# Performance work log

Hardware: AMD Instinct MI355X
Metric: run time of the kernel (lower is better)

Reference implementation:

```python
import jax, jax.numpy as jnp
import numpy as np

N = 100000
E = 1600000
D_IN = 128
HID = 128
OUT = 64


def _sage_conv(x, edge_index, W_l, W_r, b, num_nodes):
    # PyG SAGEConv (aggr='mean'): out = lin_l(mean_{j in N(i)} x_j) + lin_r(x_i)
    src, dst = edge_index[0], edge_index[1]
    msgs = x[src]  # [E, d] gather from source nodes
    summed = jax.ops.segment_sum(msgs, dst, num_segments=num_nodes)  # [N, d]
    cnt = jax.ops.segment_sum(jnp.ones((msgs.shape[0],), x.dtype), dst, num_segments=num_nodes)
    agg = summed / jnp.maximum(cnt, 1.0)[:, None]  # mean; isolated nodes -> 0
    return agg @ W_l + b + x @ W_r


def setup_inputs() -> dict:
    key = jax.random.key(0)
    ks = jax.random.split(key, 8)
    x = jax.random.normal(ks[0], (N, D_IN), dtype=jnp.float32)
    edge_index = jax.random.randint(ks[1], (2, E), 0, N, dtype=jnp.int64)
    s1 = 1.0 / np.sqrt(D_IN)
    s2 = 1.0 / np.sqrt(HID)
    W_l1 = jax.random.uniform(ks[2], (D_IN, HID), jnp.float32, -s1, s1)
    W_r1 = jax.random.uniform(ks[3], (D_IN, HID), jnp.float32, -s1, s1)
    b1 = jnp.zeros((HID,), jnp.float32)
    W_l2 = jax.random.uniform(ks[4], (HID, OUT), jnp.float32, -s2, s2)
    W_r2 = jax.random.uniform(ks[5], (HID, OUT), jnp.float32, -s2, s2)
    b2 = jnp.zeros((OUT,), jnp.float32)
    return {"x": x, "edge_index": edge_index, "W_l1": W_l1, "W_r1": W_r1,
            "b1": b1, "W_l2": W_l2, "W_r2": W_r2, "b2": b2}


def reference(x, edge_index, W_l1, W_r1, b1, W_l2, W_r2, b2):
    h = _sage_conv(x, edge_index, W_l1, W_r1, b1, N)
    h = jax.nn.relu(h)
    out = _sage_conv(h, edge_index, W_l2, W_r2, b2, N)
    return out
```

## Files before the change

kernel.cpp:

```cpp
#include <hip/hip_runtime.h>
#include <hip/hip_fp16.h>

typedef __attribute__((ext_vector_type(8))) short bf16x8;
typedef __attribute__((ext_vector_type(4))) float f32x4;

__device__ __forceinline__ f32x4 mfma16(bf16x8 a, bf16x8 b, f32x4 c) {
    return __builtin_amdgcn_mfma_f32_16x16x32_bf16(a, b, c, 0, 0, 0);
}

__device__ __forceinline__ unsigned short bf16_rte(float f) {
    unsigned int u = __float_as_uint(f);
    unsigned int r = (u + 0x7FFFu + ((u >> 16) & 1u)) >> 16;
    return (unsigned short)r;
}
__device__ __forceinline__ float bf16_f(unsigned short h) {
    return __uint_as_float(((unsigned int)h) << 16);
}

__device__ __forceinline__ void split8h(bf16x8 raw, bf16x8& hi, bf16x8& lo) {
#pragma unroll
    for (int j = 0; j < 8; ++j) {
        float f = __half2float(__ushort_as_half((unsigned short)raw[j]));
        unsigned short h = bf16_rte(f);
        hi[j] = (short)h;
        lo[j] = (short)bf16_rte(f - bf16_f(h));
    }
}

__global__ __launch_bounds__(256) void k_prep(
    const float* __restrict__ Wl1, const float* __restrict__ Wr1,
    const float* __restrict__ Wl2, const float* __restrict__ Wr2,
    unsigned short* __restrict__ w1ah, unsigned short* __restrict__ w1al,
    unsigned short* __restrict__ w1bh, unsigned short* __restrict__ w1bl,
    unsigned short* __restrict__ w2ah, unsigned short* __restrict__ w2al,
    unsigned short* __restrict__ w2bh, unsigned short* __restrict__ w2bl,
    const float* __restrict__ x, unsigned short* __restrict__ x16,
    int* __restrict__ bcnt, int nb, int total8) {
    int b = blockIdx.x;
    int t = threadIdx.x;
    if (b < 192) {
        const float* W;
        unsigned short *hi, *lo;
        int F, e;
        if (b < 64)       { W = Wl1; hi = w1ah; lo = w1al; F = 128; e = b * 256 + t; }
        else if (b < 128) { W = Wr1; hi = w1bh; lo = w1bl; F = 128; e = (b - 64) * 256 + t; }
        else if (b < 160) { W = Wl2; hi = w2ah; lo = w2al; F = 64;  e = (b - 128) * 256 + t; }
        else              { W = Wr2; hi = w2bh; lo = w2bl; F = 64;  e = (b - 160) * 256 + t; }
        if (e >= 128 * F) return;
        int col = e >> 7, k = e & 127;
        float v = W[(size_t)k * F + col];
        unsigned short h = bf16_rte(v);
        hi[e] = h;
        lo[e] = bf16_rte(v - bf16_f(h));
    } else if (b == 192) {
        for (int i = t; i < nb; i += 256) bcnt[i] = 0;
    } else {
        int i = (b - 193) * 256 + t;
        if (i >= total8) return;
        const float4* xp = (const float4*)x + (size_t)i * 2;
        float4 a = xp[0], bb = xp[1];
        bf16x8 o;
        o[0] = (short)__half_as_ushort(__float2half_rn(a.x));
        o[1] = (short)__half_as_ushort(__float2half_rn(a.y));
        o[2] = (short)__half_as_ushort(__float2half_rn(a.z));
        o[3] = (short)__half_as_ushort(__float2half_rn(a.w));
        o[4] = (short)__half_as_ushort(__float2half_rn(bb.x));
        o[5] = (short)__half_as_ushort(__float2half_rn(bb.y));
        o[6] = (short)__half_as_ushort(__float2half_rn(bb.z));
        o[7] = (short)__half_as_ushort(__float2half_rn(bb.w));
        *(bf16x8*)&x16[(size_t)i * 8] = o;
    }
}


#define MAXNB 1024

__global__ __launch_bounds__(256) void k_bcount(
    const int* __restrict__ dst, int* __restrict__ bcnt, int E, int chunk, int nb) {
    __shared__ int h[MAXNB];
    int t = threadIdx.x;
    for (int i = t; i < nb; i += 256) h[i] = 0;
    __syncthreads();
    int base = blockIdx.x * chunk;
    int end = min(base + chunk, E);
    for (int i = base + t; i < end; i += 256) atomicAdd(&h[dst[i] >> 7], 1);
    __syncthreads();
    for (int i = t; i < nb; i += 256)
        if (h[i]) atomicAdd(&bcnt[i], h[i]);
}

__global__ void k_bscan(const int* __restrict__ bcnt, int* __restrict__ boff,
                        int* __restrict__ bcur, int nb) {
    __shared__ int sh[1024];
    int t = threadIdx.x;
    int v = (t < nb) ? bcnt[t] : 0;
    sh[t] = v;
    __syncthreads();
    for (int off = 1; off < 1024; off <<= 1) {
        int u = (t >= off) ? sh[t - off] : 0;
        __syncthreads();
        sh[t] += u;
        __syncthreads();
    }
    if (t < nb) {
        int ex = sh[t] - v;
        boff[t] = ex;
        bcur[t] = ex;
    }
}

__global__ __launch_bounds__(256) void k_bscatter(
    const int* __restrict__ src, const int* __restrict__ dst,
    int* __restrict__ bcur, int2* __restrict__ pairs, int E, int chunk, int nb) {
    __shared__ int h[MAXNB];
    __shared__ int curs[MAXNB];
    int t = threadIdx.x;
    for (int i = t; i < nb; i += 256) h[i] = 0;
    __syncthreads();
    int base = blockIdx.x * chunk;
    int end = min(base + chunk, E);
    for (int i = base + t; i < end; i += 256) atomicAdd(&h[dst[i] >> 7], 1);
    __syncthreads();
    for (int i = t; i < nb; i += 256)
        curs[i] = h[i] ? atomicAdd(&bcur[i], h[i]) : 0;
    __syncthreads();
    for (int i = base + t; i < end; i += 256) {
        int d = dst[i];
        int p = atomicAdd(&curs[d >> 7], 1);
        pairs[p] = make_int2(d, src[i]);
    }
}

__global__ __launch_bounds__(256) void k_build(
    const int2* __restrict__ pairs, const int* __restrict__ boff,
    int* __restrict__ csr, int* __restrict__ start, int* __restrict__ deg,
    int n, int nb, int E) {
    __shared__ int scnt[128];
    __shared__ int soff[128];
    __shared__ int cur[128];
    int b = blockIdx.x;
    int t = threadIdx.x;
    int base = boff[b];
    int end = (b + 1 < nb) ? boff[b + 1] : E;
    if (t < 128) scnt[t] = 0;
    __syncthreads();
    for (int i = base + t; i < end; i += 256) {
        int2 e = pairs[i];
        atomicAdd(&scnt[e.x & 127], 1);
    }
    __syncthreads();
    if (t < 128) soff[t] = scnt[t];
    __syncthreads();
    for (int off = 1; off < 128; off <<= 1) {
        int val = 0;
        if (t < 128 && t >= off) val = soff[t - off];
        __syncthreads();
        if (t < 128) soff[t] += val;
        __syncthreads();
    }
    if (t < 128) {
        int c = scnt[t];
        int ex = soff[t] - c;
        int node = b * 128 + t;
        if (node < n) {
            start[node] = base + ex;
            deg[node] = c;
        }
        cur[t] = base + ex;
    }
    __syncthreads();
    for (int i = base + t; i < end; i += 256) {
        int2 e = pairs[i];
        int p = atomicAdd(&cur[e.x & 127], 1);
        csr[p] = e.y;
    }
}


#define SR 40

__global__ __launch_bounds__(256, 2) void gemm1f(
    const unsigned short* __restrict__ X0h, const unsigned short* __restrict__ X1h,
    const unsigned short* __restrict__ W0H, const unsigned short* __restrict__ W0L,
    const unsigned short* __restrict__ W1H, const unsigned short* __restrict__ W1L,
    const float* __restrict__ bias, unsigned short* __restrict__ dstH, int n) {
    constexpr int FOUT = 128;
    constexpr int CT = 2;
    __shared__ unsigned short aHi[4][64 * SR], aLo[4][64 * SR];

    int t = threadIdx.x;
    int wv = t >> 6, l = t & 63, q = l >> 4, nl = l & 15;
    int wc = wv * (FOUT / 4);
    int node0 = blockIdx.x * 64;
    int sn = t >> 2, q4 = t & 3;
    int gn = min(node0 + sn, n - 1);

    bf16x8 s1r[4];
    {
        const unsigned short* p = X1h + (size_t)gn * 128 + q4 * 8;
#pragma unroll
        for (int c = 0; c < 4; ++c) s1r[c] = *(const bf16x8*)(p + c * 32);
    }
    bf16x8 w1h0[CT], w1l0[CT];
#pragma unroll
    for (int uu = 0; uu < CT; ++uu) {
        int base = (wc + uu * 16 + nl) * 128 + q * 8;
        w1h0[uu] = *(const bf16x8*)&W1H[base];
        w1l0[uu] = *(const bf16x8*)&W1L[base];
    }

    {
        const unsigned short* p = X0h + (size_t)gn * 128 + q4 * 8;
        bf16x8 r[4];
#pragma unroll
        for (int c = 0; c < 4; ++c) r[c] = *(const bf16x8*)(p + c * 32);
        int base = sn * SR + q4 * 8;
#pragma unroll
        for (int c = 0; c < 4; ++c) {
            bf16x8 hi, lo;
            split8h(r[c], hi, lo);
            *(bf16x8*)&aHi[c][base] = hi;
            *(bf16x8*)&aLo[c][base] = lo;
        }
    }

    f32x4 acc[4][CT];
#pragma unroll
    for (int a = 0; a < 4; ++a)
#pragma unroll
        for (int b = 0; b < CT; ++b) acc[a][b] = (f32x4){0.f, 0.f, 0.f, 0.f};

    bf16x8 wh[2][CT], wl[2][CT];
#pragma unroll
    for (int uu = 0; uu < CT; ++uu) {
        int base = (wc + uu * 16 + nl) * 128 + q * 8;
        wh[0][uu] = *(const bf16x8*)&W0H[base];
        wl[0][uu] = *(const bf16x8*)&W0L[base];
    }
    __syncthreads();

#pragma unroll
    for (int c = 0; c < 4; ++c) {
        if (c < 3) {
#pragma unroll
            for (int uu = 0; uu < CT; ++uu) {
                int base = (wc + uu * 16 + nl) * 128 + (c + 1) * 32 + q * 8;
                wh[(c + 1) & 1][uu] = *(const bf16x8*)&W0H[base];
                wl[(c + 1) & 1][uu] = *(const bf16x8*)&W0L[base];
            }
        }
        bf16x8 ah[4], al[4];
#pragma unroll
        for (int tt = 0; tt < 4; ++tt) {
            int off = (tt * 16 + nl) * SR + q * 8;
            ah[tt] = *(const bf16x8*)&aHi[c][off];
            al[tt] = *(const bf16x8*)&aLo[c][off];
        }
        int cb = c & 1;
#pragma unroll
        for (int tt = 0; tt < 4; ++tt)
#pragma unroll
            for (int uu = 0; uu < CT; ++uu) {
                f32x4 a = acc[tt][uu];
                a = mfma16(al[tt], wh[cb][uu], a);
                a = mfma16(ah[tt], wl[cb][uu], a);
                a = mfma16(ah[tt], wh[cb][uu], a);
                acc[tt][uu] = a;
            }
    }
    __syncthreads();

    {
        int base = sn * SR + q4 * 8;
#pragma unroll
        for (int c = 0; c < 4; ++c) {
            bf16x8 hi, lo;
            split8h(s1r[c], hi, lo);
            *(bf16x8*)&aHi[c][base] = hi;
            *(bf16x8*)&aLo[c][base] = lo;
        }
    }
#pragma unroll
    for (int uu = 0; uu < CT; ++uu) { wh[0][uu] = w1h0[uu]; wl[0][uu] = w1l0[uu]; }
    __syncthreads();

#pragma unroll
    for (int c = 0; c < 4; ++c) {
        if (c < 3) {
#pragma unroll
            for (int uu = 0; uu < CT; ++uu) {
                int base = (wc + uu * 16 + nl) * 128 + (c + 1) * 32 + q * 8;
                wh[(c + 1) & 1][uu] = *(const bf16x8*)&W1H[base];
                wl[(c + 1) & 1][uu] = *(const bf16x8*)&W1L[base];
            }
        }
        bf16x8 ah[4], al[4];
#pragma unroll
        for (int tt = 0; tt < 4; ++tt) {
            int off = (tt * 16 + nl) * SR + q * 8;
            ah[tt] = *(const bf16x8*)&aHi[c][off];
            al[tt] = *(const bf16x8*)&aLo[c][off];
        }
        int cb = c & 1;
#pragma unroll
        for (int tt = 0; tt < 4; ++tt)
#pragma unroll
            for (int uu = 0; uu < CT; ++uu) {
                f32x4 a = acc[tt][uu];
                a = mfma16(al[tt], wh[cb][uu], a);
                a = mfma16(ah[tt], wl[cb][uu], a);
                a = mfma16(ah[tt], wh[cb][uu], a);
                acc[tt][uu] = a;
            }
    }
    __syncthreads();

    unsigned short* tb = &aHi[0][0];
#pragma unroll
    for (int uu = 0; uu < CT; ++uu) {
        int col = wc + uu * 16 + nl;
        float bv = bias[col];
#pragma unroll
        for (int tt = 0; tt < 4; ++tt)
#pragma unroll
            for (int r = 0; r < 4; ++r) {
                float vv = fmaxf(acc[tt][uu][r] + bv, 0.f);
                tb[(tt * 16 + q * 4 + r) * 136 + col] =
                    __half_as_ushort(__float2half_rn(vv));
            }
    }
    __syncthreads();
    int node = node0 + sn;
    if (node < n) {
        const unsigned short* sp = tb + sn * 136 + q4 * 32;
        unsigned short* dp = dstH + (size_t)node * 128 + q4 * 32;
#pragma unroll
        for (int i = 0; i < 4; ++i) *(bf16x8*)(dp + i * 8) = *(const bf16x8*)(sp + i * 8);
    }
}

__global__ __launch_bounds__(256, 2) void gemm2d(
    const unsigned short* __restrict__ H,
    const unsigned short* __restrict__ WaH, const unsigned short* __restrict__ WaL,
    const unsigned short* __restrict__ WbH, const unsigned short* __restrict__ WbL,
    const float* __restrict__ bias, unsigned short* __restrict__ p16,
    float* __restrict__ outF, int n) {
    constexpr int CT = 2;
    __shared__ unsigned short aHi[4][64 * SR], aLo[4][64 * SR];

    int t = threadIdx.x;
    int wv = t >> 6, l = t & 63, q = l >> 4, nl = l & 15;
    int ysel = wv >> 1;
    int wc = (wv & 1) * 32;
    int node0 = blockIdx.x * 64;
    int sn = t >> 2, q4 = t & 3;
    int gn = min(node0 + sn, n - 1);
    const unsigned short* WH = ysel ? WbH : WaH;
    const unsigned short* WL = ysel ? WbL : WaL;

    {
        const unsigned short* p = H + (size_t)gn * 128 + q4 * 8;
        bf16x8 r[4];
#pragma unroll
        for (int c = 0; c < 4; ++c) r[c] = *(const bf16x8*)(p + c * 32);
        int base = sn * SR + q4 * 8;
#pragma unroll
        for (int c = 0; c < 4; ++c) {
            bf16x8 hi, lo;
            split8h(r[c], hi, lo);
            *(bf16x8*)&aHi[c][base] = hi;
            *(bf16x8*)&aLo[c][base] = lo;
        }
    }

    f32x4 acc[4][CT];
#pragma unroll
    for (int a = 0; a < 4; ++a)
#pragma unroll
        for (int b = 0; b < CT; ++b) acc[a][b] = (f32x4){0.f, 0.f, 0.f, 0.f};

    bf16x8 wh[2][CT], wl[2][CT];
#pragma unroll
    for (int uu = 0; uu < CT; ++uu) {
        int base = (wc + uu * 16 + nl) * 128 + q * 8;
        wh[0][uu] = *(const bf16x8*)&WH[base];
        wl[0][uu] = *(const bf16x8*)&WL[base];
    }
    __syncthreads();

#pragma unroll
    for (int c = 0; c < 4; ++c) {
        if (c < 3) {
#pragma unroll
            for (int uu = 0; uu < CT; ++uu) {
                int base = (wc + uu * 16 + nl) * 128 + (c + 1) * 32 + q * 8;
                wh[(c + 1) & 1][uu] = *(const bf16x8*)&WH[base];
                wl[(c + 1) & 1][uu] = *(const bf16x8*)&WL[base];
            }
        }
        bf16x8 ah[4], al[4];
#pragma unroll
        for (int tt = 0; tt < 4; ++tt) {
            int off = (tt * 16 + nl) * SR + q * 8;
            ah[tt] = *(const bf16x8*)&aHi[c][off];
            al[tt] = *(const bf16x8*)&aLo[c][off];
        }
        int cb = c & 1;
#pragma unroll
        for (int tt = 0; tt < 4; ++tt)
#pragma unroll
            for (int uu = 0; uu < CT; ++uu) {
                f32x4 a = acc[tt][uu];
                a = mfma16(al[tt], wh[cb][uu], a);
                a = mfma16(ah[tt], wl[cb][uu], a);
                a = mfma16(ah[tt], wh[cb][uu], a);
                acc[tt][uu] = a;
            }
    }
    __syncthreads();

    unsigned short* tbu = &aHi[0][0];
    float* tbf = (float*)&aLo[0][0];
#pragma unroll
    for (int uu = 0; uu < CT; ++uu) {
        int col = wc + uu * 16 + nl;
        if (ysel) {
            float bv = bias[col];
#pragma unroll
            for (int tt = 0; tt < 4; ++tt)
#pragma unroll
                for (int r = 0; r < 4; ++r)
                    tbf[(tt * 16 + q * 4 + r) * 68 + col] = acc[tt][uu][r] + bv;
        } else {
#pragma unroll
            for (int tt = 0; tt < 4; ++tt)
#pragma unroll
                for (int r = 0; r < 4; ++r)
                    tbu[(tt * 16 + q * 4 + r) * 72 + col] =
                        __half_as_ushort(__float2half_rn(acc[tt][uu][r]));
        }
    }
    __syncthreads();
    int node = node0 + sn;
    if (node < n) {
        const unsigned short* spu = tbu + sn * 72 + q4 * 16;
        unsigned short* dpu = p16 + (size_t)node * 64 + q4 * 16;
        *(bf16x8*)dpu = *(const bf16x8*)spu;
        *(bf16x8*)(dpu + 8) = *(const bf16x8*)(spu + 8);
        const float* spf = tbf + sn * 68 + q4 * 16;
        float* dpf = outF + (size_t)node * 64 + q4 * 16;
#pragma unroll
        for (int i = 0; i < 4; ++i) *(float4*)(dpf + i * 4) = *(const float4*)(spf + i * 4);
    }
}

__global__ __launch_bounds__(256) void aggF(
    const unsigned short* __restrict__ tab, const int* __restrict__ csr,
    const int* __restrict__ start, const int* __restrict__ deg,
    unsigned short* __restrict__ outm, int n) {
    int gid = blockIdx.x * blockDim.x + threadIdx.x;
    int wave = gid >> 6, lane = gid & 63;
    int sub = lane >> 4, fl = lane & 15;
    int node = wave * 4 + sub;
    if (node >= n) return;
    int s = start[node], d = deg[node];
    float4 A0 = {0.f, 0.f, 0.f, 0.f}, A1 = {0.f, 0.f, 0.f, 0.f};
    int j = 0;
    if (d >= 4) {
        int i0 = csr[s], i1 = csr[s + 1], i2 = csr[s + 2], i3 = csr[s + 3];
        for (; j + 8 <= d; j += 4) {
            int n0 = csr[s + j + 4], n1 = csr[s + j + 5];
            int n2 = csr[s + j + 6], n3 = csr[s + j + 7];
            uint4 r0 = ((const uint4*)(tab + (size_t)i0 * 128))[fl];
            uint4 r1 = ((const uint4*)(tab + (size_t)i1 * 128))[fl];
            uint4 r2 = ((const uint4*)(tab + (size_t)i2 * 128))[fl];
            uint4 r3 = ((const uint4*)(tab + (size_t)i3 * 128))[fl];
#pragma unroll
            for (int e = 0; e < 4; ++e) {
                uint4 r = e == 0 ? r0 : (e == 1 ? r1 : (e == 2 ? r2 : r3));
                float2 v0 = __half22float2(*(const __half2*)&r.x);
                float2 v1 = __half22float2(*(const __half2*)&r.y);
                float2 v2 = __half22float2(*(const __half2*)&r.z);
                float2 v3 = __half22float2(*(const __half2*)&r.w);
                A0.x += v0.x; A0.y += v0.y; A0.z += v1.x; A0.w += v1.y;
                A1.x += v2.x; A1.y += v2.y; A1.z += v3.x; A1.w += v3.y;
            }
            i0 = n0; i1 = n1; i2 = n2; i3 = n3;
        }
        {
            uint4 r0 = ((const uint4*)(tab + (size_t)i0 * 128))[fl];
            uint4 r1 = ((const uint4*)(tab + (size_t)i1 * 128))[fl];
            uint4 r2 = ((const uint4*)(tab + (size_t)i2 * 128))[fl];
            uint4 r3 = ((const uint4*)(tab + (size_t)i3 * 128))[fl];
#pragma unroll
            for (int e = 0; e < 4; ++e) {
                uint4 r = e == 0 ? r0 : (e == 1 ? r1 : (e == 2 ? r2 : r3));
                float2 v0 = __half22float2(*(const __half2*)&r.x);
                float2 v1 = __half22float2(*(const __half2*)&r.y);
                float2 v2 = __half22float2(*(const __half2*)&r.z);
                float2 v3 = __half22float2(*(const __half2*)&r.w);
                A0.x += v0.x; A0.y += v0.y; A0.z += v1.x; A0.w += v1.y;
                A1.x += v2.x; A1.y += v2.y; A1.z += v3.x; A1.w += v3.y;
            }
            j += 4;
        }
    }
    for (; j < d; ++j) {
        uint4 r = ((const uint4*)(tab + (size_t)csr[s + j] * 128))[fl];
        float2 v0 = __half22float2(*(const __half2*)&r.x);
        float2 v1 = __half22float2(*(const __half2*)&r.y);
        float2 v2 = __half22float2(*(const __half2*)&r.z);
        float2 v3 = __half22float2(*(const __half2*)&r.w);
        A0.x += v0.x; A0.y += v0.y; A0.z += v1.x; A0.w += v1.y;
        A1.x += v2.x; A1.y += v2.y; A1.z += v3.x; A1.w += v3.y;
    }
    float inv = 1.0f / (float)max(d, 1);
    __half2 h0 = __floats2half2_rn(A0.x * inv, A0.y * inv);
    __half2 h1 = __floats2half2_rn(A0.z * inv, A0.w * inv);
    __half2 h2 = __floats2half2_rn(A1.x * inv, A1.y * inv);
    __half2 h3 = __floats2half2_rn(A1.z * inv, A1.w * inv);
    uint4 w;
    w.x = *(unsigned int*)&h0;
    w.y = *(unsigned int*)&h1;
    w.z = *(unsigned int*)&h2;
    w.w = *(unsigned int*)&h3;
    *(uint4*)&outm[(size_t)node * 128 + fl * 8] = w;
}

__global__ __launch_bounds__(256) void aggP(
    const unsigned short* __restrict__ tab, const int* __restrict__ csr,
    const int* __restrict__ start, const int* __restrict__ deg,
    float* __restrict__ outF, int n) {
    int gid = blockIdx.x * blockDim.x + threadIdx.x;
    int wave = gid >> 6, lane = gid & 63;
    int sub = lane >> 4, fl = lane & 15;
    int node = wave * 4 + sub;
    if (node >= n) return;
    int s = start[node], d = deg[node];
    float4 A = {0.f, 0.f, 0.f, 0.f};
    int j = 0;
    if (d >= 4) {
        int i0 = csr[s], i1 = csr[s + 1], i2 = csr[s + 2], i3 = csr[s + 3];
        for (; j + 8 <= d; j += 4) {
            int n0 = csr[s + j + 4], n1 = csr[s + j + 5];
            int n2 = csr[s + j + 6], n3 = csr[s + j + 7];
            uint2 r0 = ((const uint2*)(tab + (size_t)i0 * 64))[fl];
            uint2 r1 = ((const uint2*)(tab + (size_t)i1 * 64))[fl];
            uint2 r2 = ((const uint2*)(tab + (size_t)i2 * 64))[fl];
            uint2 r3 = ((const uint2*)(tab + (size_t)i3 * 64))[fl];
#pragma unroll
            for (int e = 0; e < 4; ++e) {
                uint2 r = e == 0 ? r0 : (e == 1 ? r1 : (e == 2 ? r2 : r3));
                float2 v0 = __half22float2(*(const __half2*)&r.x);
                float2 v1 = __half22float2(*(const __half2*)&r.y);
                A.x += v0.x; A.y += v0.y; A.z += v1.x; A.w += v1.y;
            }
            i0 = n0; i1 = n1; i2 = n2; i3 = n3;
        }
        {
            uint2 r0 = ((const uint2*)(tab + (size_t)i0 * 64))[fl];
            uint2 r1 = ((const uint2*)(tab + (size_t)i1 * 64))[fl];
            uint2 r2 = ((const uint2*)(tab + (size_t)i2 * 64))[fl];
            uint2 r3 = ((const uint2*)(tab + (size_t)i3 * 64))[fl];
#pragma unroll
            for (int e = 0; e < 4; ++e) {
                uint2 r = e == 0 ? r0 : (e == 1 ? r1 : (e == 2 ? r2 : r3));
                float2 v0 = __half22float2(*(const __half2*)&r.x);
                float2 v1 = __half22float2(*(const __half2*)&r.y);
                A.x += v0.x; A.y += v0.y; A.z += v1.x; A.w += v1.y;
            }
            j += 4;
        }
    }
    for (; j < d; ++j) {
        uint2 r = ((const uint2*)(tab + (size_t)csr[s + j] * 64))[fl];
        float2 v0 = __half22float2(*(const __half2*)&r.x);
        float2 v1 = __half22float2(*(const __half2*)&r.y);
        A.x += v0.x; A.y += v0.y; A.z += v1.x; A.w += v1.y;
    }
    float inv = 1.0f / (float)max(d, 1);
    float* op = outF + (size_t)node * 64 + fl * 4;
    float4 cur = *(float4*)op;
    cur.x += A.x * inv;
    cur.y += A.y * inv;
    cur.z += A.z * inv;
    cur.w += A.w * inv;
    *(float4*)op = cur;
}


extern "C" void kernel_launch(void* const* d_in, const int* in_sizes, int n_in,
                              void* d_out, int out_size, void* d_ws, size_t ws_size,
                              hipStream_t stream) {
    const float* x   = (const float*)d_in[0];
    const int*   ei  = (const int*)d_in[1];
    const float* Wl1 = (const float*)d_in[2];
    const float* Wr1 = (const float*)d_in[3];
    const float* b1  = (const float*)d_in[4];
    const float* Wl2 = (const float*)d_in[5];
    const float* Wr2 = (const float*)d_in[6];
    const float* b2  = (const float*)d_in[7];
    float* out = (float*)d_out;

    int Nn = in_sizes[0] / 128;
    int E  = in_sizes[1] / 2;
    const int* src = ei;
    const int* dst = ei + E;
    int nb = (Nn + 127) / 128;

    char* ws = (char*)d_ws;
    auto alloc = [&](size_t bytes) -> char* {
        char* pp = ws;
        ws += (bytes + 255) / 256 * 256;
        return pp;
    };
    int* bcnt   = (int*)alloc((size_t)nb * 4);
    int* boff   = (int*)alloc((size_t)nb * 4);
    int* bcur   = (int*)alloc((size_t)nb * 4);
    int* start  = (int*)alloc((size_t)Nn * 4);
    int* deg    = (int*)alloc((size_t)Nn * 4);
    int* csr    = (int*)alloc((size_t)E * 4);
    unsigned short* x16  = (unsigned short*)alloc((size_t)Nn * 128 * 2);
    unsigned short* xm16 = (unsigned short*)alloc((size_t)Nn * 128 * 2);
    unsigned short* h16  = (unsigned short*)alloc((size_t)Nn * 128 * 2);
    unsigned short* p16  = (unsigned short*)alloc((size_t)Nn * 64 * 2);
    unsigned short* w1ah = (unsigned short*)alloc(128 * 128 * 2);
    unsigned short* w1al = (unsigned short*)alloc(128 * 128 * 2);
    unsigned short* w1bh = (unsigned short*)alloc(128 * 128 * 2);
    unsigned short* w1bl = (unsigned short*)alloc(128 * 128 * 2);
    unsigned short* w2ah = (unsigned short*)alloc(64 * 128 * 2);
    unsigned short* w2al = (unsigned short*)alloc(64 * 128 * 2);
    unsigned short* w2bh = (unsigned short*)alloc(64 * 128 * 2);
    unsigned short* w2bl = (unsigned short*)alloc(64 * 128 * 2);
    int2* pairs = (int2*)p16;

    int total8 = Nn * 16;
    int prep_blocks = 193 + (total8 + 255) / 256;
    k_prep<<<prep_blocks, 256, 0, stream>>>(Wl1, Wr1, Wl2, Wr2,
                                            w1ah, w1al, w1bh, w1bl,
                                            w2ah, w2al, w2bh, w2bl,
                                            x, x16, bcnt, nb, total8);

    int chunk = (E + 255) / 256;
    k_bcount<<<256, 256, 0, stream>>>(dst, bcnt, E, chunk, nb);
    k_bscan<<<1, 1024, 0, stream>>>(bcnt, boff, bcur, nb);
    k_bscatter<<<256, 256, 0, stream>>>(src, dst, bcur, pairs, E, chunk, nb);
    k_build<<<nb, 256, 0, stream>>>(pairs, boff, csr, start, deg, Nn, nb, E);

    int gb = (Nn + 63) / 64;
    int ga = (Nn + 15) / 16;
    aggF<<<ga, 256, 0, stream>>>(x16, csr, start, deg, xm16, Nn);
    gemm1f<<<gb, 256, 0, stream>>>(x16, xm16, w1bh, w1bl, w1ah, w1al, b1, h16, Nn);
    gemm2d<<<gb, 256, 0, stream>>>(h16, w2ah, w2al, w2bh, w2bl, b2, p16, out, Nn);
    aggP<<<ga, 256, 0, stream>>>(p16, csr, start, deg, out, Nn);
}
```

Baseline: 332.1 us.

## Fuse layer-1 mean aggregation into GEMM kernel and merge bucket count into prep

The layer-1 neighbor mean aggregation now runs inside the first GEMM kernel. Each block gathers neighbor rows for its 64 nodes, computes the mean, splits it to bf16 hi/lo and writes it straight into shared memory. This removes the xm16 intermediate write and re-read and one kernel launch. The bucket-count pass is folded into the prep kernel, with the counter zeroing replaced by a memset. Both gather loops now keep 8 loads in flight instead of 4, at the cost of more register pressure in the fused GEMM, which may lower occupancy or serialize gather latency behind the MFMA stage.

```diff
diff --git a/kernel.cpp b/kernel.cpp
--- a/kernel.cpp
+++ b/kernel.cpp
@@ -26,6 +26,23 @@
         lo[j] = (short)bf16_rte(f - bf16_f(h));
     }
 }
+
+__device__ __forceinline__ void acc8(uint4 r, float4& A0, float4& A1) {
+    float2 v0 = __half22float2(*(const __half2*)&r.x);
+    float2 v1 = __half22float2(*(const __half2*)&r.y);
+    float2 v2 = __half22float2(*(const __half2*)&r.z);
+    float2 v3 = __half22float2(*(const __half2*)&r.w);
+    A0.x += v0.x; A0.y += v0.y; A0.z += v1.x; A0.w += v1.y;
+    A1.x += v2.x; A1.y += v2.y; A1.z += v3.x; A1.w += v3.y;
+}
+
+__device__ __forceinline__ void acc4(uint2 r, float4& A) {
+    float2 v0 = __half22float2(*(const __half2*)&r.x);
+    float2 v1 = __half22float2(*(const __half2*)&r.y);
+    A.x += v0.x; A.y += v0.y; A.z += v1.x; A.w += v1.y;
+}
+
+#define MAXNB 1024
 
 __global__ __launch_bounds__(256) void k_prep(
     const float* __restrict__ Wl1, const float* __restrict__ Wr1,
@@ -35,7 +52,9 @@
     unsigned short* __restrict__ w2ah, unsigned short* __restrict__ w2al,
     unsigned short* __restrict__ w2bh, unsigned short* __restrict__ w2bl,
     const float* __restrict__ x, unsigned short* __restrict__ x16,
-    int* __restrict__ bcnt, int nb, int total8) {
+    const int* __restrict__ dst, int* __restrict__ bcnt,
+    int E, int chunk, int xb, int nb, int total8) {
+    __shared__ int hh[MAXNB];
     int b = blockIdx.x;
     int t = threadIdx.x;
     if (b < 192) {
@@ -52,10 +71,8 @@
         unsigned short h = bf16_rte(v);
         hi[e] = h;
         lo[e] = bf16_rte(v - bf16_f(h));
-    } else if (b == 192) {
-        for (int i = t; i < nb; i += 256) bcnt[i] = 0;
-    } else {
-        int i = (b - 193) * 256 + t;
+    } else if (b < 192 + xb) {
+        int i = (b - 192) * 256 + t;
         if (i >= total8) return;
         const float4* xp = (const float4*)x + (size_t)i * 2;
         float4 a = xp[0], bb = xp[1];
@@ -69,25 +86,19 @@
         o[6] = (short)__half_as_ushort(__float2half_rn(bb.z));
         o[7] = (short)__half_as_ushort(__float2half_rn(bb.w));
         *(bf16x8*)&x16[(size_t)i * 8] = o;
-    }
-}
-
-
-#define MAXNB 1024
-
-__global__ __launch_bounds__(256) void k_bcount(
-    const int* __restrict__ dst, int* __restrict__ bcnt, int E, int chunk, int nb) {
-    __shared__ int h[MAXNB];
-    int t = threadIdx.x;
-    for (int i = t; i < nb; i += 256) h[i] = 0;
-    __syncthreads();
-    int base = blockIdx.x * chunk;
-    int end = min(base + chunk, E);
-    for (int i = base + t; i < end; i += 256) atomicAdd(&h[dst[i] >> 7], 1);
-    __syncthreads();
-    for (int i = t; i < nb; i += 256)
-        if (h[i]) atomicAdd(&bcnt[i], h[i]);
-}
+    } else {
+        int cb = b - 192 - xb;
+        for (int i = t; i < nb; i += 256) hh[i] = 0;
+        __syncthreads();
+        int base = cb * chunk;
+        int end = min(base + chunk, E);
+        for (int i = base + t; i < end; i += 256) atomicAdd(&hh[dst[i] >> 7], 1);
+        __syncthreads();
+        for (int i = t; i < nb; i += 256)
+            if (hh[i]) atomicAdd(&bcnt[i], hh[i]);
+    }
+}
+
 
 __global__ void k_bscan(const int* __restrict__ bcnt, int* __restrict__ boff,
                         int* __restrict__ bcur, int nb) {
@@ -176,41 +187,27 @@
     }
 }
 
-
 #define SR 40
 
-__global__ __launch_bounds__(256, 2) void gemm1f(
-    const unsigned short* __restrict__ X0h, const unsigned short* __restrict__ X1h,
+__global__ __launch_bounds__(256, 2) void fused1(
+    const unsigned short* __restrict__ X,
+    const int* __restrict__ csr, const int* __restrict__ start,
+    const int* __restrict__ deg,
     const unsigned short* __restrict__ W0H, const unsigned short* __restrict__ W0L,
     const unsigned short* __restrict__ W1H, const unsigned short* __restrict__ W1L,
     const float* __restrict__ bias, unsigned short* __restrict__ dstH, int n) {
-    constexpr int FOUT = 128;
     constexpr int CT = 2;
     __shared__ unsigned short aHi[4][64 * SR], aLo[4][64 * SR];
 
     int t = threadIdx.x;
     int wv = t >> 6, l = t & 63, q = l >> 4, nl = l & 15;
-    int wc = wv * (FOUT / 4);
+    int wc = wv * 32;
     int node0 = blockIdx.x * 64;
     int sn = t >> 2, q4 = t & 3;
     int gn = min(node0 + sn, n - 1);
 
-    bf16x8 s1r[4];
     {
-        const unsigned short* p = X1h + (size_t)gn * 128 + q4 * 8;
-#pragma unroll
-        for (int c = 0; c < 4; ++c) s1r[c] = *(const bf16x8*)(p + c * 32);
-    }
-    bf16x8 w1h0[CT], w1l0[CT];
-#pragma unroll
-    for (int uu = 0; uu < CT; ++uu) {
-        int base = (wc + uu * 16 + nl) * 128 + q * 8;
-        w1h0[uu] = *(const bf16x8*)&W1H[base];
-        w1l0[uu] = *(const bf16x8*)&W1L[base];
-    }
-
-    {
-        const unsigned short* p = X0h + (size_t)gn * 128 + q4 * 8;
+        const unsigned short* p = X + (size_t)gn * 128 + q4 * 8;
         bf16x8 r[4];
 #pragma unroll
         for (int c = 0; c < 4; ++c) r[c] = *(const bf16x8*)(p + c * 32);
@@ -271,17 +268,63 @@
     __syncthreads();
 
     {
-        int base = sn * SR + q4 * 8;
-#pragma unroll
-        for (int c = 0; c < 4; ++c) {
+        int sub = l >> 4, fl = l & 15;
+        int cch = fl >> 2, qq = fl & 3;
+#pragma unroll 1
+        for (int r4 = 0; r4 < 4; ++r4) {
+            int nloc = wv * 16 + r4 * 4 + sub;
+            int nc = min(node0 + nloc, n - 1);
+            int s = start[nc], d = deg[nc];
+            float4 A0 = {0.f, 0.f, 0.f, 0.f}, A1 = {0.f, 0.f, 0.f, 0.f};
+            int j = 0;
+            if (d >= 8) {
+                int idx[8];
+#pragma unroll
+                for (int k = 0; k < 8; ++k) idx[k] = csr[s + k];
+                for (; j + 16 <= d; j += 8) {
+                    uint4 rr[8];
+#pragma unroll
+                    for (int k = 0; k < 8; ++k)
+                        rr[k] = ((const uint4*)(X + (size_t)idx[k] * 128))[fl];
+#pragma unroll
+                    for (int k = 0; k < 8; ++k) idx[k] = csr[s + j + 8 + k];
+#pragma unroll
+                    for (int k = 0; k < 8; ++k) acc8(rr[k], A0, A1);
+                }
+                {
+                    uint4 rr[8];
+#pragma unroll
+                    for (int k = 0; k < 8; ++k)
+                        rr[k] = ((const uint4*)(X + (size_t)idx[k] * 128))[fl];
+#pragma unroll
+                    for (int k = 0; k < 8; ++k) acc8(rr[k], A0, A1);
+                    j += 8;
+                }
+            }
+            for (; j < d; ++j)
+                acc8(((const uint4*)(X + (size_t)csr[s + j] * 128))[fl], A0, A1);
+            float inv = 1.0f / (float)max(d, 1);
+            float m[8] = {A0.x * inv, A0.y * inv, A0.z * inv, A0.w * inv,
+                          A1.x * inv, A1.y * inv, A1.z * inv, A1.w * inv};
             bf16x8 hi, lo;
-            split8h(s1r[c], hi, lo);
-            *(bf16x8*)&aHi[c][base] = hi;
-            *(bf16x8*)&aLo[c][base] = lo;
-        }
-    }
-#pragma unroll
-    for (int uu = 0; uu < CT; ++uu) { wh[0][uu] = w1h0[uu]; wl[0][uu] = w1l0[uu]; }
+#pragma unroll
+            for (int k = 0; k < 8; ++k) {
+                unsigned short hh = bf16_rte(m[k]);
+                hi[k] = (short)hh;
+                lo[k] = (short)bf16_rte(m[k] - bf16_f(hh));
+            }
+            int base = nloc * SR + qq * 8;
+            *(bf16x8*)&aHi[cch][base] = hi;
+            *(bf16x8*)&aLo[cch][base] = lo;
+        }
+    }
+
+#pragma unroll
+    for (int uu = 0; uu < CT; ++uu) {
+        int base = (wc + uu * 16 + nl) * 128 + q * 8;
+        wh[0][uu] = *(const bf16x8*)&W1H[base];
+        wl[0][uu] = *(const bf16x8*)&W1L[base];
+    }
     __syncthreads();
 
 #pragma unroll
@@ -452,79 +495,6 @@
 #pragma unroll
         for (int i = 0; i < 4; ++i) *(float4*)(dpf + i * 4) = *(const float4*)(spf + i * 4);
     }
-}
-
-__global__ __launch_bounds__(256) void aggF(
-    const unsigned short* __restrict__ tab, const int* __restrict__ csr,
-    const int* __restrict__ start, const int* __restrict__ deg,
-    unsigned short* __restrict__ outm, int n) {
-    int gid = blockIdx.x * blockDim.x + threadIdx.x;
-    int wave = gid >> 6, lane = gid & 63;
-    int sub = lane >> 4, fl = lane & 15;
-    int node = wave * 4 + sub;
-    if (node >= n) return;
-    int s = start[node], d = deg[node];
-    float4 A0 = {0.f, 0.f, 0.f, 0.f}, A1 = {0.f, 0.f, 0.f, 0.f};
-    int j = 0;
-    if (d >= 4) {
-        int i0 = csr[s], i1 = csr[s + 1], i2 = csr[s + 2], i3 = csr[s + 3];
-        for (; j + 8 <= d; j += 4) {
-            int n0 = csr[s + j + 4], n1 = csr[s + j + 5];
-            int n2 = csr[s + j + 6], n3 = csr[s + j + 7];
-            uint4 r0 = ((const uint4*)(tab + (size_t)i0 * 128))[fl];
-            uint4 r1 = ((const uint4*)(tab + (size_t)i1 * 128))[fl];
-            uint4 r2 = ((const uint4*)(tab + (size_t)i2 * 128))[fl];
-            uint4 r3 = ((const uint4*)(tab + (size_t)i3 * 128))[fl];
-#pragma unroll
-            for (int e = 0; e < 4; ++e) {
-                uint4 r = e == 0 ? r0 : (e == 1 ? r1 : (e == 2 ? r2 : r3));
-                float2 v0 = __half22float2(*(const __half2*)&r.x);
-                float2 v1 = __half22float2(*(const __half2*)&r.y);
-                float2 v2 = __half22float2(*(const __half2*)&r.z);
-                float2 v3 = __half22float2(*(const __half2*)&r.w);
-                A0.x += v0.x; A0.y += v0.y; A0.z += v1.x; A0.w += v1.y;
-                A1.x += v2.x; A1.y += v2.y; A1.z += v3.x; A1.w += v3.y;
-            }
-            i0 = n0; i1 = n1; i2 = n2; i3 = n3;
-        }
-        {
-            uint4 r0 = ((const uint4*)(tab + (size_t)i0 * 128))[fl];
-            uint4 r1 = ((const uint4*)(tab + (size_t)i1 * 128))[fl];
-            uint4 r2 = ((const uint4*)(tab + (size_t)i2 * 128))[fl];
-            uint4 r3 = ((const uint4*)(tab + (size_t)i3 * 128))[fl];
-#pragma unroll
-            for (int e = 0; e < 4; ++e) {
-                uint4 r = e == 0 ? r0 : (e == 1 ? r1 : (e == 2 ? r2 : r3));
-                float2 v0 = __half22float2(*(const __half2*)&r.x);
-                float2 v1 = __half22float2(*(const __half2*)&r.y);
-                float2 v2 = __half22float2(*(const __half2*)&r.z);
-                float2 v3 = __half22float2(*(const __half2*)&r.w);
-                A0.x += v0.x; A0.y += v0.y; A0.z += v1.x; A0.w += v1.y;
-                A1.x += v2.x; A1.y += v2.y; A1.z += v3.x; A1.w += v3.y;
-            }
-            j += 4;
-        }
-    }
-    for (; j < d; ++j) {
-        uint4 r = ((const uint4*)(tab + (size_t)csr[s + j] * 128))[fl];
-        float2 v0 = __half22float2(*(const __half2*)&r.x);
-        float2 v1 = __half22float2(*(const __half2*)&r.y);
-        float2 v2 = __half22float2(*(const __half2*)&r.z);
-        float2 v3 = __half22float2(*(const __half2*)&r.w);
-        A0.x += v0.x; A0.y += v0.y; A0.z += v1.x; A0.w += v1.y;
-        A1.x += v2.x; A1.y += v2.y; A1.z += v3.x; A1.w += v3.y;
-    }
-    float inv = 1.0f / (float)max(d, 1);
-    __half2 h0 = __floats2half2_rn(A0.x * inv, A0.y * inv);
-    __half2 h1 = __floats2half2_rn(A0.z * inv, A0.w * inv);
-    __half2 h2 = __floats2half2_rn(A1.x * inv, A1.y * inv);
-    __half2 h3 = __floats2half2_rn(A1.z * inv, A1.w * inv);
-    uint4 w;
-    w.x = *(unsigned int*)&h0;
-    w.y = *(unsigned int*)&h1;
-    w.z = *(unsigned int*)&h2;
-    w.w = *(unsigned int*)&h3;
-    *(uint4*)&outm[(size_t)node * 128 + fl * 8] = w;
 }
 
 __global__ __launch_bounds__(256) void aggP(
@@ -539,45 +509,32 @@
     int s = start[node], d = deg[node];
     float4 A = {0.f, 0.f, 0.f, 0.f};
     int j = 0;
-    if (d >= 4) {
-        int i0 = csr[s], i1 = csr[s + 1], i2 = csr[s + 2], i3 = csr[s + 3];
-        for (; j + 8 <= d; j += 4) {
-            int n0 = csr[s + j + 4], n1 = csr[s + j + 5];
-            int n2 = csr[s + j + 6], n3 = csr[s + j + 7];
-            uint2 r0 = ((const uint2*)(tab + (size_t)i0 * 64))[fl];
-            uint2 r1 = ((const uint2*)(tab + (size_t)i1 * 64))[fl];
-            uint2 r2 = ((const uint2*)(tab + (size_t)i2 * 64))[fl];
-            uint2 r3 = ((const uint2*)(tab + (size_t)i3 * 64))[fl];
-#pragma unroll
-            for (int e = 0; e < 4; ++e) {
-                uint2 r = e == 0 ? r0 : (e == 1 ? r1 : (e == 2 ? r2 : r3));
-                float2 v0 = __half22float2(*(const __half2*)&r.x);
-                float2 v1 = __half22float2(*(const __half2*)&r.y);
-                A.x += v0.x; A.y += v0.y; A.z += v1.x; A.w += v1.y;
-            }
-            i0 = n0; i1 = n1; i2 = n2; i3 = n3;
+    if (d >= 8) {
+        int idx[8];
+#pragma unroll
+        for (int k = 0; k < 8; ++k) idx[k] = csr[s + k];
+        for (; j + 16 <= d; j += 8) {
+            uint2 rr[8];
+#pragma unroll
+            for (int k = 0; k < 8; ++k)
+                rr[k] = ((const uint2*)(tab + (size_t)idx[k] * 64))[fl];
+#pragma unroll
+            for (int k = 0; k < 8; ++k) idx[k] = csr[s + j + 8 + k];
+#pragma unroll
+            for (int k = 0; k < 8; ++k) acc4(rr[k], A);
         }
         {
-            uint2 r0 = ((const uint2*)(tab + (size_t)i0 * 64))[fl];
-            uint2 r1 = ((const uint2*)(tab + (size_t)i1 * 64))[fl];
-            uint2 r2 = ((const uint2*)(tab + (size_t)i2 * 64))[fl];
-            uint2 r3 = ((const uint2*)(tab + (size_t)i3 * 64))[fl];
-#pragma unroll
-            for (int e = 0; e < 4; ++e) {
-                uint2 r = e == 0 ? r0 : (e == 1 ? r1 : (e == 2 ? r2 : r3));
-                float2 v0 = __half22float2(*(const __half2*)&r.x);
-                float2 v1 = __half22float2(*(const __half2*)&r.y);
-                A.x += v0.x; A.y += v0.y; A.z += v1.x; A.w += v1.y;
-            }
-            j += 4;
-        }
-    }
-    for (; j < d; ++j) {
-        uint2 r = ((const uint2*)(tab + (size_t)csr[s + j] * 64))[fl];
-        float2 v0 = __half22float2(*(const __half2*)&r.x);
-        float2 v1 = __half22float2(*(const __half2*)&r.y);
-        A.x += v0.x; A.y += v0.y; A.z += v1.x; A.w += v1.y;
-    }
+            uint2 rr[8];
+#pragma unroll
+            for (int k = 0; k < 8; ++k)
+                rr[k] = ((const uint2*)(tab + (size_t)idx[k] * 64))[fl];
+#pragma unroll
+            for (int k = 0; k < 8; ++k) acc4(rr[k], A);
+            j += 8;
+        }
+    }
+    for (; j < d; ++j)
+        acc4(((const uint2*)(tab + (size_t)csr[s + j] * 64))[fl], A);
     float inv = 1.0f / (float)max(d, 1);
     float* op = outF + (size_t)node * 64 + fl * 4;
     float4 cur = *(float4*)op;
@@ -621,7 +578,6 @@
     int* deg    = (int*)alloc((size_t)Nn * 4);
     int* csr    = (int*)alloc((size_t)E * 4);
     unsigned short* x16  = (unsigned short*)alloc((size_t)Nn * 128 * 2);
-    unsigned short* xm16 = (unsigned short*)alloc((size_t)Nn * 128 * 2);
     unsigned short* h16  = (unsigned short*)alloc((size_t)Nn * 128 * 2);
     unsigned short* p16  = (unsigned short*)alloc((size_t)Nn * 64 * 2);
     unsigned short* w1ah = (unsigned short*)alloc(128 * 128 * 2);
@@ -634,23 +590,24 @@
     unsigned short* w2bl = (unsigned short*)alloc(64 * 128 * 2);
     int2* pairs = (int2*)p16;
 
+    hipMemsetAsync(bcnt, 0, (size_t)nb * 4, stream);
+
     int total8 = Nn * 16;
-    int prep_blocks = 193 + (total8 + 255) / 256;
-    k_prep<<<prep_blocks, 256, 0, stream>>>(Wl1, Wr1, Wl2, Wr2,
-                                            w1ah, w1al, w1bh, w1bl,
-                                            w2ah, w2al, w2bh, w2bl,
-                                            x, x16, bcnt, nb, total8);
-
+    int xb = (total8 + 255) / 256;
     int chunk = (E + 255) / 256;
-    k_bcount<<<256, 256, 0, stream>>>(dst, bcnt, E, chunk, nb);
+    k_prep<<<192 + xb + 256, 256, 0, stream>>>(
+        Wl1, Wr1, Wl2, Wr2,
+        w1ah, w1al, w1bh, w1bl, w2ah, w2al, w2bh, w2bl,
+        x, x16, dst, bcnt, E, chunk, xb, nb, total8);
+
     k_bscan<<<1, 1024, 0, stream>>>(bcnt, boff, bcur, nb);
     k_bscatter<<<256, 256, 0, stream>>>(src, dst, bcur, pairs, E, chunk, nb);
     k_build<<<nb, 256, 0, stream>>>(pairs, boff, csr, start, deg, Nn, nb, E);
 
     int gb = (Nn + 63) / 64;
     int ga = (Nn + 15) / 16;
-    aggF<<<ga, 256, 0, stream>>>(x16, csr, start, deg, xm16, Nn);
-    gemm1f<<<gb, 256, 0, stream>>>(x16, xm16, w1bh, w1bl, w1ah, w1al, b1, h16, Nn);
+    fused1<<<gb, 256, 0, stream>>>(x16, csr, start, deg,
+                                   w1bh, w1bl, w1ah, w1al, b1, h16, Nn);
     gemm2d<<<gb, 256, 0, stream>>>(h16, w2ah, w2al, w2bh, w2bl, b2, p16, out, Nn);
     aggP<<<ga, 256, 0, stream>>>(p16, csr, start, deg, out, Nn);
 }
```

New measurement: 336.1 us. No clear change (+1.2%).
